# Kernel optimization log

Measured on AMD Instinct MI355X. Metric: run time of the kernel, lower is better.

## Reference

```python
import jax, jax.numpy as jnp
import numpy as np
import math

B, S, H, OUT = 8, 2048, 512, 512
NQ, NL = 8, 3            # num_qubits, num_layers
NP = NQ // 2             # entangled pairs = 4
PS = H // NP             # pair size = 128
NS = NQ                  # superposition states = 8

_H2 = jnp.array([[1.0, 1.0], [1.0, -1.0]], jnp.float32) / math.sqrt(2.0)
_PX = jnp.array([[0.0, 1.0], [1.0, 0.0]], jnp.float32)
_PZ = jnp.array([[1.0, 0.0], [0.0, -1.0]], jnp.float32)
_CNOT = jnp.array([[1, 0, 0, 0], [0, 1, 0, 0], [0, 0, 0, 1], [0, 0, 1, 0]], jnp.float32)


def _gate2(x, m):
    # apply a 2x2 gate to consecutive pairs along the last dim
    shp = x.shape
    return (x.reshape(shp[:-1] + (shp[-1] // 2, 2)) @ m).reshape(shp)


def _cnot(x):
    # apply 4x4 CNOT to consecutive quadruples along the last dim
    shp = x.shape
    return (x.reshape(shp[:-1] + (shp[-1] // 4, 4)) @ _CNOT).reshape(shp)


def setup_inputs() -> dict:
    key = jax.random.key(0)
    ks = jax.random.split(key, 8)
    x = jax.random.normal(ks[0], (B, S, H), jnp.float32)
    in_W = jax.random.normal(ks[1], (H, H), jnp.float32) / math.sqrt(H)
    in_b = jnp.zeros((H,), jnp.float32)
    ent_W = jax.random.normal(ks[2], (NP, PS, PS), jnp.float32) * 0.1
    ent_strength = jnp.ones((NP,), jnp.float32)
    sup_W = jax.random.normal(ks[3], (NS, H), jnp.float32) * 0.1
    sup_coeffs = jnp.ones((NS,), jnp.float32) / math.sqrt(NS)
    circuit_params = jax.random.normal(ks[4], (NL, NQ, 3), jnp.float32) * 0.1
    meas_ops = jnp.eye(H, dtype=jnp.float32)  # 'computational' basis
    out_W = jax.random.normal(ks[5], (H, OUT), jnp.float32) / math.sqrt(H)
    out_b = jnp.zeros((OUT,), jnp.float32)
    return dict(x=x, in_W=in_W, in_b=in_b, ent_W=ent_W, ent_strength=ent_strength,
                sup_W=sup_W, sup_coeffs=sup_coeffs, circuit_params=circuit_params,
                meas_ops=meas_ops, out_W=out_W, out_b=out_b)


def reference(x, in_W, in_b, ent_W, ent_strength, sup_W, sup_coeffs,
              circuit_params, meas_ops, out_W, out_b):
    # input projection
    x = x @ in_W + in_b

    # quantum entanglement: per-pair linear map + CNOT + strength scale
    xp = x.reshape(B, S, NP, PS)
    xp = jnp.einsum('bspi,pij->bspj', xp, ent_W)
    xp = _cnot(xp) * ent_strength[None, None, :, None]
    x = xp.reshape(B, S, H)

    # quantum superposition: the Hadamard gate is identical across states,
    # so sum_i coeff_i * w_i * Had(x) = Had(x) * sum_i coeff_i * w_i
    x = _gate2(x, _H2) * jnp.einsum('s,sh->h', sup_coeffs, sup_W)

    # variational circuit layers
    rep = H // NQ  # tile per-qubit params across hidden
    for layer in range(NL):
        x = _gate2(x, _H2)
        px = jnp.repeat(circuit_params[layer, :, 0], rep)
        x = x + px * _gate2(x, _PX)
        # Pauli-Y branch: (x + 0j) @ [[0,-i],[i,0]] is purely imaginary ->
        # its real part is exactly zero; faithful no-op (zero grads too)
        pz = jnp.repeat(circuit_params[layer, :, 2], rep)
        x = x + pz * _gate2(x, _PZ)
        x = _cnot(x)

    # measurement (computational basis) + output projection
    x = x @ meas_ops
    return x @ out_W + out_b


if __name__ == '__main__':
    out = reference(**setup_inputs())
    print(out.shape, out.dtype)
```

## Files before the change

kernel.cpp:

```cpp
#include <hip/hip_runtime.h>
#include <hip/hip_bf16.h>


typedef float  fvec4 __attribute__((ext_vector_type(4)));
typedef float  f32x4 __attribute__((ext_vector_type(4)));
typedef short  short8 __attribute__((ext_vector_type(8)));
typedef unsigned short us8 __attribute__((ext_vector_type(8)));
typedef unsigned short us4 __attribute__((ext_vector_type(4)));

#define H 512
#define NL 3

__device__ __forceinline__ unsigned short f2bf(float f) {
    return __bfloat16_as_ushort(__float2bfloat16(f));
}
__device__ __forceinline__ float bf2f(unsigned short u) {
    return __uint_as_float((unsigned int)u << 16);
}
__device__ __forceinline__ void gll16(const void* g, void* l) {
    __builtin_amdgcn_global_load_lds((const __attribute__((address_space(1))) void*)g,
                                     (__attribute__((address_space(3))) void*)l, 16, 0, 0);
}
__device__ __forceinline__ int swz1024(int r, int byte) {
    return r * 1024 + (((byte >> 4) ^ (r & 7)) << 4) + (byte & 15);
}

__global__ __launch_bounds__(512) void k_prep(const float* __restrict__ in_W,
                                              const float* __restrict__ in_b,
                                              const float* __restrict__ entW,
                                              const float* __restrict__ strength,
                                              const float* __restrict__ supW,
                                              const float* __restrict__ coeffs,
                                              const float* __restrict__ cp,
                                              float* __restrict__ W1f,
                                              float* __restrict__ bvec) {
    __shared__ float sseg[H];
    __shared__ float sval[H];
    __shared__ float sw[H];
    const int r = blockIdx.x;
    const int tid = threadIdx.x;
    const float* src = (r < H) ? (in_W + (size_t)r * H) : in_b;
    float* dst = (r < H) ? (W1f + (size_t)r * H) : bvec;

    sseg[tid] = src[tid];
    float wacc = 0.f;
#pragma unroll
    for (int s = 0; s < 8; ++s) wacc += coeffs[s] * supW[s * H + tid];
    sw[tid] = wacc;
    __syncthreads();

    const int p = tid >> 7, j = tid & 127;
    const int jsrc = (j & 2) ? (j ^ 1) : j;
    const float* wcol = entW + p * (128 * 128) + jsrc;
    const float* seg = sseg + p * 128;
    float acc = 0.f;
#pragma unroll 8
    for (int i = 0; i < 128; ++i) acc += seg[i] * wcol[i * 128];
    acc *= strength[p];
    __syncthreads();
    sval[tid] = acc;
    __syncthreads();

    const float is2 = 0.70710678118654752440f;
    const int q4 = tid & ~3;
    float v0 = sval[q4], v1 = sval[q4 + 1], v2 = sval[q4 + 2], v3 = sval[q4 + 3];
    float t0, t1, t2, t3;
    t0 = (v0 + v1) * is2; t1 = (v0 - v1) * is2;
    t2 = (v2 + v3) * is2; t3 = (v2 - v3) * is2;
    v0 = t0 * sw[q4]; v1 = t1 * sw[q4 + 1]; v2 = t2 * sw[q4 + 2]; v3 = t3 * sw[q4 + 3];
    const int qb = tid >> 6;
#pragma unroll
    for (int l = 0; l < NL; ++l) {
        float px = cp[l * 24 + qb * 3 + 0];
        float pz = cp[l * 24 + qb * 3 + 2];
        t0 = (v0 + v1) * is2; t1 = (v0 - v1) * is2;
        t2 = (v2 + v3) * is2; t3 = (v2 - v3) * is2;
        v0 = t0; v1 = t1; v2 = t2; v3 = t3;
        t0 = v0 + px * v1; t1 = v1 + px * v0;
        t2 = v2 + px * v3; t3 = v3 + px * v2;
        v0 = t0; v1 = t1; v2 = t2; v3 = t3;
        v0 *= (1.f + pz); v1 *= (1.f - pz);
        v2 *= (1.f + pz); v3 *= (1.f - pz);
        t0 = v2; v2 = v3; v3 = t0;
    }
    const int pos = tid & 3;
    dst[tid] = (pos == 0) ? v0 : (pos == 1) ? v1 : (pos == 2) ? v2 : v3;
}

__global__ __launch_bounds__(512) void k_mid(const float* __restrict__ W1f,
                                             const float* __restrict__ outW,
                                             const float* __restrict__ bvec,
                                             const float* __restrict__ outb,
                                             unsigned short* __restrict__ MtotT,
                                             float* __restrict__ btot) {
    __shared__ __align__(16) char smem[65536];
    const int bx = blockIdx.x;
    const int tid = threadIdx.x;

    char* As = smem;
    char* Bs = smem + 32768;
    const int bm = (bx >> 4) * 32, bn = (bx & 15) * 32;

#pragma unroll
    for (int i = 0; i < 4; ++i) {
        int c = i * 512 + tid;
        int m = c >> 6, kc = (c & 63) * 8;
        const float* s = W1f + (size_t)(bm + m) * H + kc;
        fvec4 a0 = *(const fvec4*)s, a1 = *(const fvec4*)(s + 4);
        us8 hv;
        hv[0] = f2bf(a0.x); hv[1] = f2bf(a0.y); hv[2] = f2bf(a0.z); hv[3] = f2bf(a0.w);
        hv[4] = f2bf(a1.x); hv[5] = f2bf(a1.y); hv[6] = f2bf(a1.z); hv[7] = f2bf(a1.w);
        *(us8*)(As + swz1024(m, kc * 2)) = hv;
    }
#pragma unroll
    for (int i = 0; i < 8; ++i) {
        int c = i * 512 + tid;
        int k = c >> 3, n4 = (c & 7) * 4;
        fvec4 v = *(const fvec4*)(outW + (size_t)k * H + bn + n4);
#pragma unroll
        for (int jj = 0; jj < 4; ++jj) {
            int n = n4 + jj;
            float vv = (jj == 0) ? v.x : (jj == 1) ? v.y : (jj == 2) ? v.z : v.w;
            *(unsigned short*)(Bs + swz1024(n, k * 2)) = f2bf(vv);
        }
    }
    __syncthreads();

    const int lane = tid & 63, w = tid >> 6;
    if (w < 4) {
        const int ro = lane & 15, ko8 = (lane >> 4) * 8;
        const int crow = (lane >> 4) * 4, ccol = lane & 15;
        const int mt = w >> 1, nt = w & 1;
        f32x4 acc = (f32x4)0.f;
#pragma unroll
        for (int ks = 0; ks < 16; ++ks) {
            const int kb = (ks * 32 + ko8) * 2;
            short8 af = *(const short8*)(As + swz1024(mt * 16 + ro, kb));
            short8 bf = *(const short8*)(Bs + swz1024(nt * 16 + ro, kb));
            acc = __builtin_amdgcn_mfma_f32_16x16x32_bf16(af, bf, acc, 0, 0, 0);
        }
        const int gcol = bn + nt * 16 + ccol;
        us4 hv;
        hv[0] = f2bf(acc[0]); hv[1] = f2bf(acc[1]);
        hv[2] = f2bf(acc[2]); hv[3] = f2bf(acc[3]);
        *(us4*)(MtotT + (size_t)gcol * H + bm + mt * 16 + crow) = hv;
    }

    if (bx < 16) {
        const int n = tid >> 4;
        const int ks = tid & 15;
        float part = 0.f;
#pragma unroll 8
        for (int i = 0; i < 32; ++i) {
            const int k = ks * 32 + i;
            unsigned short u = *(const unsigned short*)(Bs + swz1024(n, k * 2));
            part += bvec[k] * bf2f(u);
        }
        part += __shfl_xor(part, 1, 16);
        part += __shfl_xor(part, 2, 16);
        part += __shfl_xor(part, 4, 16);
        part += __shfl_xor(part, 8, 16);
        if (ks == 0) btot[bn + n] = part + outb[bn + n];
    }
}

__global__ __launch_bounds__(512, 4) void k_main(const float* __restrict__ A,
                                                 const unsigned short* __restrict__ Bt,
                                                 float* __restrict__ C,
                                                 const float* __restrict__ bias) {
    __shared__ __align__(16) unsigned short As[2][64 * 64];
    __shared__ __align__(16) unsigned short Bs[2][256 * 64];
    const int tid = threadIdx.x;
    const int bm = blockIdx.x * 64;
    const int bn = blockIdx.y * 256;
    const int lane = tid & 63, wid = tid >> 6;
    const int ro = lane & 15, ko8 = (lane >> 4) * 8;

    const int arr = tid >> 3, akc = (tid & 7) * 8;
    const float* aptr = A + (size_t)(bm + arr) * H + akc;
    const int awoff = ((arr * 128 + akc * 2) ^ ((arr & 7) << 4));

    const int brow = tid >> 3;
    const char* bbase = (const char*)Bt + (size_t)(bn + brow) * 1024 +
                        (((tid & 7) * 16) ^ ((brow & 7) << 4));
    const int bdst = wid * 1024;

    f32x4 acc[4][2];
#pragma unroll
    for (int i = 0; i < 4; ++i)
#pragma unroll
        for (int j = 0; j < 2; ++j) acc[i][j] = (f32x4)0.f;

    {
        fvec4 a0 = *(const fvec4*)aptr, a1 = *(const fvec4*)(aptr + 4);
#pragma unroll
        for (int i = 0; i < 4; ++i)
            gll16(bbase + (size_t)i * 65536, (char*)&Bs[0][0] + i * 8192 + bdst);
        us8 hv;
        hv[0] = f2bf(a0.x); hv[1] = f2bf(a0.y); hv[2] = f2bf(a0.z); hv[3] = f2bf(a0.w);
        hv[4] = f2bf(a1.x); hv[5] = f2bf(a1.y); hv[6] = f2bf(a1.z); hv[7] = f2bf(a1.w);
        *(us8*)((char*)&As[0][0] + awoff) = hv;
    }
    __syncthreads();

    for (int t = 0; t < 8; ++t) {
        const int buf = t & 1;
        fvec4 pa0, pa1;
        if (t < 7) {
            pa0 = *(const fvec4*)(aptr + (t + 1) * 64);
            pa1 = *(const fvec4*)(aptr + (t + 1) * 64 + 4);
#pragma unroll
            for (int i = 0; i < 4; ++i)
                gll16(bbase + (size_t)i * 65536 + (t + 1) * 128,
                      (char*)&Bs[buf ^ 1][0] + i * 8192 + bdst);
        }
#pragma unroll
        for (int kk = 0; kk < 2; ++kk) {
            short8 af[4], bfr[2];
#pragma unroll
            for (int am = 0; am < 4; ++am) {
                int row = am * 16 + ro;
                af[am] = *(const short8*)((const char*)&As[buf][0] +
                         ((row * 128 + (kk * 32 + ko8) * 2) ^ ((row & 7) << 4)));
            }
#pragma unroll
            for (int bj = 0; bj < 2; ++bj) {
                int row = wid * 32 + bj * 16 + ro;
                bfr[bj] = *(const short8*)((const char*)&Bs[buf][0] +
                          ((row * 128 + (kk * 32 + ko8) * 2) ^ ((row & 7) << 4)));
            }
#pragma unroll
            for (int am = 0; am < 4; ++am)
#pragma unroll
                for (int bj = 0; bj < 2; ++bj)
                    acc[am][bj] = __builtin_amdgcn_mfma_f32_16x16x32_bf16(af[am], bfr[bj], acc[am][bj], 0, 0, 0);
        }
        if (t < 7) {
            us8 hv;
            hv[0] = f2bf(pa0.x); hv[1] = f2bf(pa0.y); hv[2] = f2bf(pa0.z); hv[3] = f2bf(pa0.w);
            hv[4] = f2bf(pa1.x); hv[5] = f2bf(pa1.y); hv[6] = f2bf(pa1.z); hv[7] = f2bf(pa1.w);
            *(us8*)((char*)&As[buf ^ 1][0] + awoff) = hv;
        }
        __syncthreads();
    }

    const int crow = (lane >> 4) * 4, ccol = lane & 15;
#pragma unroll
    for (int am = 0; am < 4; ++am)
#pragma unroll
        for (int bj = 0; bj < 2; ++bj) {
            const int gcol = bn + wid * 32 + bj * 16 + ccol;
            const float bv = bias[gcol];
            const int grow = bm + am * 16 + crow;
#pragma unroll
            for (int j = 0; j < 4; ++j)
                C[(size_t)(grow + j) * H + gcol] = acc[am][bj][j] + bv;
        }
}

extern "C" void kernel_launch(void* const* d_in, const int* in_sizes, int n_in,
                              void* d_out, int out_size, void* d_ws, size_t ws_size,
                              hipStream_t stream) {
    const float* x      = (const float*)d_in[0];
    const float* in_W   = (const float*)d_in[1];
    const float* in_b   = (const float*)d_in[2];
    const float* ent_W  = (const float*)d_in[3];
    const float* ent_s  = (const float*)d_in[4];
    const float* sup_W  = (const float*)d_in[5];
    const float* sup_c  = (const float*)d_in[6];
    const float* cp     = (const float*)d_in[7];
    const float* out_W  = (const float*)d_in[9];
    const float* out_b  = (const float*)d_in[10];
    float* out = (float*)d_out;

    char* ws = (char*)d_ws;
    const size_t MB = 1u << 20;
    if (ws_size < 16384 + MB + MB) return;

    float* btot = (float*)(ws);
    float* bvec = (float*)(ws + 4096);
    float* W1f  = (float*)(ws + 16384);
    unsigned short* MtotT = (unsigned short*)(ws + 16384 + MB);

    k_prep<<<dim3(513), dim3(512), 0, stream>>>(in_W, in_b, ent_W, ent_s, sup_W,
                                                sup_c, cp, W1f, bvec);
    k_mid<<<dim3(256), dim3(512), 0, stream>>>(W1f, out_W, bvec, out_b, MtotT, btot);
    k_main<<<dim3(256, 2), dim3(512), 0, stream>>>(x, MtotT, out, btot);
}
```

Measured before the change: 37.93 us.

## Halve k_main N-tile for more blocks and pack two rows per k_prep block

k_main now computes 64x128 output tiles instead of 64x256, so each wave does 4 MFMAs per k-step and the grid grows to 256x4 blocks with a higher occupancy hint. The aim is better spread across compute units and lower LDS use per block, at the cost of loading each A tile twice as often. k_prep now handles two weight rows per 512-thread block (256 blocks instead of 513), with the bias row done in a second pass by block 0. Its inner dot product is split over four accumulators to shorten the add dependency chain.

```diff
diff --git a/kernel.cpp b/kernel.cpp
--- a/kernel.cpp
+++ b/kernel.cpp
@@ -34,57 +34,82 @@
                                               const float* __restrict__ cp,
                                               float* __restrict__ W1f,
                                               float* __restrict__ bvec) {
-    __shared__ float sseg[H];
-    __shared__ float sval[H];
+    __shared__ float sseg[2][H];
+    __shared__ float sval[2][H];
     __shared__ float sw[H];
-    const int r = blockIdx.x;
+    const int bx = blockIdx.x;
     const int tid = threadIdx.x;
-    const float* src = (r < H) ? (in_W + (size_t)r * H) : in_b;
-    float* dst = (r < H) ? (W1f + (size_t)r * H) : bvec;
-
-    sseg[tid] = src[tid];
+    const float is2 = 0.70710678118654752440f;
+
     float wacc = 0.f;
 #pragma unroll
     for (int s = 0; s < 8; ++s) wacc += coeffs[s] * supW[s * H + tid];
     sw[tid] = wacc;
-    __syncthreads();
-
-    const int p = tid >> 7, j = tid & 127;
-    const int jsrc = (j & 2) ? (j ^ 1) : j;
-    const float* wcol = entW + p * (128 * 128) + jsrc;
-    const float* seg = sseg + p * 128;
-    float acc = 0.f;
-#pragma unroll 8
-    for (int i = 0; i < 128; ++i) acc += seg[i] * wcol[i * 128];
-    acc *= strength[p];
-    __syncthreads();
-    sval[tid] = acc;
-    __syncthreads();
-
-    const float is2 = 0.70710678118654752440f;
-    const int q4 = tid & ~3;
-    float v0 = sval[q4], v1 = sval[q4 + 1], v2 = sval[q4 + 2], v3 = sval[q4 + 3];
-    float t0, t1, t2, t3;
-    t0 = (v0 + v1) * is2; t1 = (v0 - v1) * is2;
-    t2 = (v2 + v3) * is2; t3 = (v2 - v3) * is2;
-    v0 = t0 * sw[q4]; v1 = t1 * sw[q4 + 1]; v2 = t2 * sw[q4 + 2]; v3 = t3 * sw[q4 + 3];
-    const int qb = tid >> 6;
-#pragma unroll
-    for (int l = 0; l < NL; ++l) {
-        float px = cp[l * 24 + qb * 3 + 0];
-        float pz = cp[l * 24 + qb * 3 + 2];
-        t0 = (v0 + v1) * is2; t1 = (v0 - v1) * is2;
-        t2 = (v2 + v3) * is2; t3 = (v2 - v3) * is2;
-        v0 = t0; v1 = t1; v2 = t2; v3 = t3;
-        t0 = v0 + px * v1; t1 = v1 + px * v0;
-        t2 = v2 + px * v3; t3 = v3 + px * v2;
-        v0 = t0; v1 = t1; v2 = t2; v3 = t3;
-        v0 *= (1.f + pz); v1 *= (1.f - pz);
-        v2 *= (1.f + pz); v3 *= (1.f - pz);
-        t0 = v2; v2 = v3; v3 = t0;
-    }
-    const int pos = tid & 3;
-    dst[tid] = (pos == 0) ? v0 : (pos == 1) ? v1 : (pos == 2) ? v2 : v3;
+    const int half = tid >> 8, t = tid & 255;
+
+    for (int pass = 0; pass < 2; ++pass) {
+        const bool active = (pass == 0) || (bx == 0 && half == 0);
+        const int r = 2 * bx + half;
+        const float* src = (pass == 0) ? (in_W + (size_t)r * H) : in_b;
+        float* dst = (pass == 0) ? (W1f + (size_t)r * H) : bvec;
+        __syncthreads();
+        if (active) {
+            sseg[half][t] = src[t];
+            sseg[half][256 + t] = src[256 + t];
+        }
+        __syncthreads();
+        if (active) {
+#pragma unroll
+            for (int cc = 0; cc < 2; ++cc) {
+                const int c = t + cc * 256;
+                const int p = c >> 7, j = c & 127;
+                const int jsrc = (j & 2) ? (j ^ 1) : j;
+                const float* wcol = entW + p * 16384 + jsrc;
+                const float* seg = &sseg[half][p * 128];
+                float a0 = 0.f, a1 = 0.f, a2 = 0.f, a3 = 0.f;
+#pragma unroll 4
+                for (int i = 0; i < 128; i += 4) {
+                    a0 += seg[i + 0] * wcol[(i + 0) * 128];
+                    a1 += seg[i + 1] * wcol[(i + 1) * 128];
+                    a2 += seg[i + 2] * wcol[(i + 2) * 128];
+                    a3 += seg[i + 3] * wcol[(i + 3) * 128];
+                }
+                sval[half][c] = ((a0 + a1) + (a2 + a3)) * strength[p];
+            }
+        }
+        __syncthreads();
+        if (active) {
+#pragma unroll
+            for (int cc = 0; cc < 2; ++cc) {
+                const int c = t + cc * 256;
+                const int q4 = c & ~3;
+                float v0 = sval[half][q4], v1 = sval[half][q4 + 1];
+                float v2 = sval[half][q4 + 2], v3 = sval[half][q4 + 3];
+                float t0, t1, t2, t3;
+                t0 = (v0 + v1) * is2; t1 = (v0 - v1) * is2;
+                t2 = (v2 + v3) * is2; t3 = (v2 - v3) * is2;
+                v0 = t0 * sw[q4]; v1 = t1 * sw[q4 + 1];
+                v2 = t2 * sw[q4 + 2]; v3 = t3 * sw[q4 + 3];
+                const int qb = c >> 6;
+#pragma unroll
+                for (int l = 0; l < NL; ++l) {
+                    float px = cp[l * 24 + qb * 3 + 0];
+                    float pz = cp[l * 24 + qb * 3 + 2];
+                    t0 = (v0 + v1) * is2; t1 = (v0 - v1) * is2;
+                    t2 = (v2 + v3) * is2; t3 = (v2 - v3) * is2;
+                    v0 = t0; v1 = t1; v2 = t2; v3 = t3;
+                    t0 = v0 + px * v1; t1 = v1 + px * v0;
+                    t2 = v2 + px * v3; t3 = v3 + px * v2;
+                    v0 = t0; v1 = t1; v2 = t2; v3 = t3;
+                    v0 *= (1.f + pz); v1 *= (1.f - pz);
+                    v2 *= (1.f + pz); v3 *= (1.f - pz);
+                    t0 = v2; v2 = v3; v3 = t0;
+                }
+                const int pos = c & 3;
+                dst[c] = (pos == 0) ? v0 : (pos == 1) ? v1 : (pos == 2) ? v2 : v3;
+            }
+        }
+    }
 }
 
 __global__ __launch_bounds__(512) void k_mid(const float* __restrict__ W1f,
@@ -164,15 +189,15 @@
     }
 }
 
-__global__ __launch_bounds__(512, 4) void k_main(const float* __restrict__ A,
+__global__ __launch_bounds__(512, 6) void k_main(const float* __restrict__ A,
                                                  const unsigned short* __restrict__ Bt,
                                                  float* __restrict__ C,
                                                  const float* __restrict__ bias) {
     __shared__ __align__(16) unsigned short As[2][64 * 64];
-    __shared__ __align__(16) unsigned short Bs[2][256 * 64];
+    __shared__ __align__(16) unsigned short Bs[2][128 * 64];
     const int tid = threadIdx.x;
     const int bm = blockIdx.x * 64;
-    const int bn = blockIdx.y * 256;
+    const int bn = blockIdx.y * 128;
     const int lane = tid & 63, wid = tid >> 6;
     const int ro = lane & 15, ko8 = (lane >> 4) * 8;
 
@@ -185,16 +210,14 @@
                         (((tid & 7) * 16) ^ ((brow & 7) << 4));
     const int bdst = wid * 1024;
 
-    f32x4 acc[4][2];
-#pragma unroll
-    for (int i = 0; i < 4; ++i)
-#pragma unroll
-        for (int j = 0; j < 2; ++j) acc[i][j] = (f32x4)0.f;
+    f32x4 acc[4];
+#pragma unroll
+    for (int i = 0; i < 4; ++i) acc[i] = (f32x4)0.f;
 
     {
         fvec4 a0 = *(const fvec4*)aptr, a1 = *(const fvec4*)(aptr + 4);
 #pragma unroll
-        for (int i = 0; i < 4; ++i)
+        for (int i = 0; i < 2; ++i)
             gll16(bbase + (size_t)i * 65536, (char*)&Bs[0][0] + i * 8192 + bdst);
         us8 hv;
         hv[0] = f2bf(a0.x); hv[1] = f2bf(a0.y); hv[2] = f2bf(a0.z); hv[3] = f2bf(a0.w);
@@ -210,30 +233,27 @@
             pa0 = *(const fvec4*)(aptr + (t + 1) * 64);
             pa1 = *(const fvec4*)(aptr + (t + 1) * 64 + 4);
 #pragma unroll
-            for (int i = 0; i < 4; ++i)
+            for (int i = 0; i < 2; ++i)
                 gll16(bbase + (size_t)i * 65536 + (t + 1) * 128,
                       (char*)&Bs[buf ^ 1][0] + i * 8192 + bdst);
         }
 #pragma unroll
         for (int kk = 0; kk < 2; ++kk) {
-            short8 af[4], bfr[2];
+            short8 af[4], bfr;
 #pragma unroll
             for (int am = 0; am < 4; ++am) {
                 int row = am * 16 + ro;
                 af[am] = *(const short8*)((const char*)&As[buf][0] +
                          ((row * 128 + (kk * 32 + ko8) * 2) ^ ((row & 7) << 4)));
             }
-#pragma unroll
-            for (int bj = 0; bj < 2; ++bj) {
-                int row = wid * 32 + bj * 16 + ro;
-                bfr[bj] = *(const short8*)((const char*)&Bs[buf][0] +
-                          ((row * 128 + (kk * 32 + ko8) * 2) ^ ((row & 7) << 4)));
+            {
+                int row = wid * 16 + ro;
+                bfr = *(const short8*)((const char*)&Bs[buf][0] +
+                      ((row * 128 + (kk * 32 + ko8) * 2) ^ ((row & 7) << 4)));
             }
 #pragma unroll
             for (int am = 0; am < 4; ++am)
-#pragma unroll
-                for (int bj = 0; bj < 2; ++bj)
-                    acc[am][bj] = __builtin_amdgcn_mfma_f32_16x16x32_bf16(af[am], bfr[bj], acc[am][bj], 0, 0, 0);
+                acc[am] = __builtin_amdgcn_mfma_f32_16x16x32_bf16(af[am], bfr, acc[am], 0, 0, 0);
         }
         if (t < 7) {
             us8 hv;
@@ -246,16 +266,14 @@
 
     const int crow = (lane >> 4) * 4, ccol = lane & 15;
 #pragma unroll
-    for (int am = 0; am < 4; ++am)
-#pragma unroll
-        for (int bj = 0; bj < 2; ++bj) {
-            const int gcol = bn + wid * 32 + bj * 16 + ccol;
-            const float bv = bias[gcol];
-            const int grow = bm + am * 16 + crow;
-#pragma unroll
-            for (int j = 0; j < 4; ++j)
-                C[(size_t)(grow + j) * H + gcol] = acc[am][bj][j] + bv;
-        }
+    for (int am = 0; am < 4; ++am) {
+        const int gcol = bn + wid * 16 + ccol;
+        const float bv = bias[gcol];
+        const int grow = bm + am * 16 + crow;
+#pragma unroll
+        for (int j = 0; j < 4; ++j)
+            C[(size_t)(grow + j) * H + gcol] = acc[am][j] + bv;
+    }
 }
 
 extern "C" void kernel_launch(void* const* d_in, const int* in_sizes, int n_in,
@@ -282,8 +300,8 @@
     float* W1f  = (float*)(ws + 16384);
     unsigned short* MtotT = (unsigned short*)(ws + 16384 + MB);
 
-    k_prep<<<dim3(513), dim3(512), 0, stream>>>(in_W, in_b, ent_W, ent_s, sup_W,
+    k_prep<<<dim3(256), dim3(512), 0, stream>>>(in_W, in_b, ent_W, ent_s, sup_W,
                                                 sup_c, cp, W1f, bvec);
     k_mid<<<dim3(256), dim3(512), 0, stream>>>(W1f, out_W, bvec, out_b, MtotT, btot);
-    k_main<<<dim3(256, 2), dim3(512), 0, stream>>>(x, MtotT, out, btot);
-}
+    k_main<<<dim3(256, 4), dim3(512), 0, stream>>>(x, MtotT, out, btot);
+}
```

Result: slower. 48.38 us (+27.5%).
